# Optimization experiments

Hardware: AMD Instinct MI355X
Metric: run time of the kernel (lower is better)

Reference implementation:

```python
import jax, jax.numpy as jnp
import numpy as np

B, T, D, U = 32, 2048, 1024, 1024


def setup_inputs() -> dict:
    key = jax.random.key(0)
    ks = jax.random.split(key, 6)
    scale = 0.02
    return {
        "query": jax.random.normal(ks[0], (B, D), jnp.float32),
        "values": jax.random.normal(ks[1], (B, T, D), jnp.float32),
        "W1_k": jax.random.normal(ks[2], (D, U), jnp.float32) * scale,
        "W1_b": jnp.zeros((U,), jnp.float32),
        "W2_k": jax.random.normal(ks[3], (D, U), jnp.float32) * scale,
        "W2_b": jnp.zeros((U,), jnp.float32),
        "V_k": jax.random.normal(ks[4], (U, 1), jnp.float32) * scale,
        "V_b": jnp.zeros((1,), jnp.float32),
    }


def reference(query, values, W1_k, W1_b, W2_k, W2_b, V_k, V_b):
    # query: [B, D] -> [B, 1, U]; values: [B, T, D] -> [B, T, U]
    q_proj = (query @ W1_k + W1_b)[:, None, :]
    v_proj = jnp.einsum("btd,du->btu", values, W2_k) + W2_b
    # score: [B, T, 1]
    score = jnp.tanh(q_proj + v_proj) @ V_k + V_b
    attention_weights = jax.nn.softmax(score, axis=1)  # over time axis T
    context_vector = jnp.sum(attention_weights * values, axis=1)  # [B, D]
    return context_vector
```

## Files before the change

### kernel.cpp

```cpp
#include <hip/hip_runtime.h>

#define NB 32
#define NT 2048
#define ND 1024
#define NU 1024
#define NM (NB*NT)

using f32x4 = __attribute__((ext_vector_type(4))) float;
using s16x8 = __attribute__((ext_vector_type(8))) short;

#define BAR()   asm volatile("s_barrier" ::: "memory")
#define LGKM0() asm volatile("s_waitcnt lgkmcnt(0)" ::: "memory")
#define VMC(n)  asm volatile("s_waitcnt vmcnt(" #n ")" ::: "memory")
#define SB0()   __builtin_amdgcn_sched_barrier(0)

__device__ __forceinline__ unsigned short f2bf(float f) {
  unsigned u = __builtin_bit_cast(unsigned, f);
  u = u + 0x7fffu + ((u >> 16) & 1u);
  return (unsigned short)(u >> 16);
}

__device__ __forceinline__ unsigned cvtpk(float lo, float hi) {
  unsigned r;
  asm("v_cvt_pk_bf16_f32 %0, %1, %2" : "=v"(r) : "v"(lo), "v"(hi));
  return r;
}

__device__ __forceinline__ void gload_lds16(const void* g, void* l) {
  __builtin_amdgcn_global_load_lds(
      (const __attribute__((address_space(1))) unsigned int*)g,
      (__attribute__((address_space(3))) unsigned int*)l, 16, 0, 0);
}

__device__ __forceinline__ float tanh_fast(float x) {
  float e = __expf(2.0f * x);
  return 1.0f - 2.0f * __builtin_amdgcn_rcpf(e + 1.0f);
}

__device__ __forceinline__ void stage_half(const unsigned short* g, int gk,
                                           unsigned short* l, int w, int r3, int c8s) {
#pragma unroll
  for (int i = 0; i < 2; ++i) {
    int cb = i * 8 + w;
    gload_lds16(g + (((size_t)(cb * 8 + r3)) << 10) + gk + c8s * 8, l + cb * 512);
  }
}

__device__ __forceinline__ void load_halfA(const float* g, int kbase, int arow, int acol,
                                           float4 (&f)[4]) {
  const float* p = g + ((size_t)arow << 10) + kbase + acol * 16;
  f[0] = *(const float4*)(p);
  f[1] = *(const float4*)(p + 4);
  f[2] = *(const float4*)(p + 8);
  f[3] = *(const float4*)(p + 12);
}

__device__ __forceinline__ void cvt_half(const float4 (&f)[4], unsigned (&pk)[8]) {
  pk[0] = cvtpk(f[0].x, f[0].y); pk[1] = cvtpk(f[0].z, f[0].w);
  pk[2] = cvtpk(f[1].x, f[1].y); pk[3] = cvtpk(f[1].z, f[1].w);
  pk[4] = cvtpk(f[2].x, f[2].y); pk[5] = cvtpk(f[2].z, f[2].w);
  pk[6] = cvtpk(f[3].x, f[3].y); pk[7] = cvtpk(f[3].z, f[3].w);
}

__device__ __forceinline__ void write_half(const unsigned (&pk)[8], unsigned short* lds,
                                           int row, int acol) {
  int r7 = row & 7;
  int c0 = (acol * 2) ^ r7, c1 = (acol * 2 + 1) ^ r7;
  *(uint4*)(lds + (row << 6) + c0 * 8) = make_uint4(pk[0], pk[1], pk[2], pk[3]);
  *(uint4*)(lds + (row << 6) + c1 * 8) = make_uint4(pk[4], pk[5], pk[6], pk[7]);
}

#define MFMA_Q(MB, NB2) \
  _Pragma("unroll") \
  for (int m = 0; m < 4; ++m) { \
    _Pragma("unroll") \
    for (int n = 0; n < 2; ++n) { \
      _Pragma("unroll") \
      for (int ks = 0; ks < 2; ++ks) \
        acc[(MB) + m][(NB2) + n] = __builtin_amdgcn_mfma_f32_16x16x32_bf16( \
            fa[m][ks], fb[(NB2) + n][ks], acc[(MB) + m][(NB2) + n], 0, 0, 0); \
    } \
  }

template<bool ACVT, bool AISS, bool BST>
__device__ __forceinline__ void tile_body(
    int kt, int buf, const float* gA, const unsigned short* gB,
    unsigned short* sA, unsigned short* sB, f32x4 (&acc)[8][4], float4 (&ah)[2][4],
    int w, int wr, int wc, int l15, int lg, int r3, int c8s, int arow, int acol) {
  const unsigned short* pA = sA + buf * 16384;
  const unsigned short* pB = sB + buf * 16384;
  unsigned short* wA = sA + (buf ^ 1) * 16384;
  unsigned short* nB = sB + buf * 16384;
  const int l7 = l15 & 7;
  s16x8 fa[4][2], fb[4][2];
#pragma unroll
  for (int m = 0; m < 4; ++m)
#pragma unroll
    for (int ks = 0; ks < 2; ++ks)
      fa[m][ks] = *(const s16x8*)(pA + ((wr * 128 + m * 16 + l15) << 6) + (((ks * 4 + lg) ^ l7) << 3));
#pragma unroll
  for (int n = 0; n < 4; ++n)
#pragma unroll
    for (int ks = 0; ks < 2; ++ks)
      fb[n][ks] = *(const s16x8*)(pB + ((wc * 64 + n * 16 + l15) << 6) + (((ks * 4 + lg) ^ l7) << 3));
  BAR(); LGKM0(); SB0();
  __builtin_amdgcn_s_setprio(1); MFMA_Q(0, 0); __builtin_amdgcn_s_setprio(0);
  BAR();
  if (ACVT) {
    unsigned pk[8];
    cvt_half(ah[0], pk);
    write_half(pk, wA, arow, acol);
  }
  if (BST) stage_half(gB, (kt + 2) * 64, nB, w, r3, c8s);
  __builtin_amdgcn_s_setprio(1); MFMA_Q(0, 2); __builtin_amdgcn_s_setprio(0);
  LGKM0();
  BAR();
#pragma unroll
  for (int m = 0; m < 4; ++m)
#pragma unroll
    for (int ks = 0; ks < 2; ++ks)
      fa[m][ks] = *(const s16x8*)(pA + ((wr * 128 + (4 + m) * 16 + l15) << 6) + (((ks * 4 + lg) ^ l7) << 3));
  if (ACVT) {
    unsigned pk[8];
    cvt_half(ah[1], pk);
    write_half(pk, wA, 128 + arow, acol);
  }
  if (AISS) load_halfA(gA, (kt + 2) * 64, arow, acol, ah[0]);
  if (BST) stage_half(gB + (128 << 10), (kt + 2) * 64, nB + 8192, w, r3, c8s);
  LGKM0(); SB0();
  __builtin_amdgcn_s_setprio(1); MFMA_Q(4, 0); __builtin_amdgcn_s_setprio(0);
  BAR();
  if (AISS) load_halfA(gA + (128 << 10), (kt + 2) * 64, arow, acol, ah[1]);
  __builtin_amdgcn_s_setprio(1); MFMA_Q(4, 2); __builtin_amdgcn_s_setprio(0);
  BAR();
}

__global__ __launch_bounds__(512, 2) void k_score_gemm8(
    const float* __restrict__ values, const unsigned short* __restrict__ W2t,
    const float* __restrict__ add2, const float* __restrict__ Vk,
    float* __restrict__ score_part) {
  __shared__ unsigned short sA[32768];
  __shared__ unsigned short sB[32768];
  const int tid = threadIdx.x;
  const int w = tid >> 6, lane = tid & 63;
  const int wr = w >> 2, wc = w & 3;
  const int l15 = lane & 15, lg = lane >> 4;
  const int r3 = lane >> 3, c8s = (lane & 7) ^ r3;
  const int arow = tid >> 2, acol = tid & 3;

  const int L = blockIdx.x;
  const int g = (L & 7) * 128 + (L >> 3);
  const int mtile = g >> 2, ntile = g & 3;

  const float* gA = values + ((size_t)mtile << 18);
  const unsigned short* gB = W2t + ((size_t)ntile << 18);

  f32x4 acc[8][4] = {};
  float4 ah[2][4];

  {
    float4 f0[4], f1[4];
    unsigned p0[8], p1[8];
    load_halfA(gA, 0, arow, acol, f0);
    load_halfA(gA + (128 << 10), 0, arow, acol, f1);
    cvt_half(f0, p0); cvt_half(f1, p1);
    write_half(p0, sA, arow, acol);
    write_half(p1, sA, 128 + arow, acol);
    stage_half(gB, 0, sB, w, r3, c8s);
    stage_half(gB + (128 << 10), 0, sB + 8192, w, r3, c8s);
    stage_half(gB, 64, sB + 16384, w, r3, c8s);
    stage_half(gB + (128 << 10), 64, sB + 16384 + 8192, w, r3, c8s);
    load_halfA(gA, 64, arow, acol, ah[0]);
    load_halfA(gA + (128 << 10), 64, arow, acol, ah[1]);
    VMC(8);
    LGKM0();
    BAR();
  }

  int buf = 0;
  for (int kt = 0; kt < 14; ++kt) {
    tile_body<true, true, true>(kt, buf, gA, gB, sA, sB, acc, ah, w, wr, wc, l15, lg, r3, c8s, arow, acol);
    buf ^= 1;
  }
  tile_body<true, false, false>(14, buf, gA, gB, sA, sB, acc, ah, w, wr, wc, l15, lg, r3, c8s, arow, acol);
  buf ^= 1;
  tile_body<false, false, false>(15, buf, gA, gB, sA, sB, acc, ah, w, wr, wc, l15, lg, r3, c8s, arow, acol);

  const int b = (mtile * 256) >> 11;
  float vks[4], adds[4];
#pragma unroll
  for (int n = 0; n < 4; ++n) {
    int u = ntile * 256 + wc * 64 + n * 16 + l15;
    vks[n] = Vk[u];
    adds[n] = add2[(b << 10) + u];
  }
  __syncthreads();
  float* part = (float*)sA;
#pragma unroll
  for (int m = 0; m < 8; ++m) {
#pragma unroll
    for (int j = 0; j < 4; ++j) {
      float s = 0.f;
#pragma unroll
      for (int n = 0; n < 4; ++n) {
        float x = acc[m][n][j] + adds[n];
        s = fmaf(tanh_fast(x), vks[n], s);
      }
#pragma unroll
      for (int off = 1; off < 16; off <<= 1) s += __shfl_xor(s, off);
      if (l15 == 0) part[wc * 256 + wr * 128 + m * 16 + lg * 4 + j] = s;
    }
  }
  __syncthreads();
  if (tid < 256) {
    float v = part[tid] + part[256 + tid] + part[512 + tid] + part[768 + tid];
    score_part[((size_t)ntile << 16) + mtile * 256 + tid] = v;
  }
}

__global__ void k_qproj(const float* __restrict__ q, const float* __restrict__ W1,
                        const float* __restrict__ W1b, const float* __restrict__ W2b,
                        float* __restrict__ add2) {
  int u = blockIdx.x * 256 + threadIdx.x;
  int b = blockIdx.y;
  const float* qr = q + (b << 10);
  float s = 0.f;
#pragma unroll 8
  for (int d = 0; d < ND; ++d) s = fmaf(qr[d], W1[d * NU + u], s);
  add2[(b << 10) + u] = s + W1b[u] + W2b[u];
}

__global__ void k_w2t(const float* __restrict__ W2, unsigned short* __restrict__ W2t) {
  __shared__ unsigned short tile[64][65];
  int bu = blockIdx.x * 64, bd = blockIdx.y * 64;
  int x = threadIdx.x & 63, y4 = threadIdx.x >> 6;
#pragma unroll
  for (int r = 0; r < 16; ++r) {
    int dl = y4 * 16 + r;
    tile[x][dl] = f2bf(W2[(size_t)(bd + dl) * NU + bu + x]);
  }
  __syncthreads();
#pragma unroll
  for (int r = 0; r < 16; ++r) {
    int ul = y4 * 16 + r;
    W2t[(size_t)(bu + ul) * ND + bd + x] = tile[ul][x];
  }
}

__global__ void k_softmax(const float* __restrict__ sp, float* __restrict__ w) {
  __shared__ float redm[4], reds[4];
  int b = blockIdx.x, tid = threadIdx.x;
  float s[8];
  float mx = -1e30f;
#pragma unroll
  for (int i = 0; i < 8; ++i) {
    int t = i * 256 + tid;
    float v = 0.f;
#pragma unroll
    for (int p = 0; p < 4; ++p) v += sp[((size_t)p << 16) + (b << 11) + t];
    s[i] = v;
    mx = fmaxf(mx, v);
  }
#pragma unroll
  for (int o = 1; o < 64; o <<= 1) mx = fmaxf(mx, __shfl_xor(mx, o));
  if ((tid & 63) == 0) redm[tid >> 6] = mx;
  __syncthreads();
  mx = fmaxf(fmaxf(redm[0], redm[1]), fmaxf(redm[2], redm[3]));
  float sum = 0.f;
#pragma unroll
  for (int i = 0; i < 8; ++i) { s[i] = __expf(s[i] - mx); sum += s[i]; }
#pragma unroll
  for (int o = 1; o < 64; o <<= 1) sum += __shfl_xor(sum, o);
  if ((tid & 63) == 0) reds[tid >> 6] = sum;
  __syncthreads();
  float inv = 1.0f / (reds[0] + reds[1] + reds[2] + reds[3]);
#pragma unroll
  for (int i = 0; i < 8; ++i) w[(b << 11) + i * 256 + tid] = s[i] * inv;
}

__global__ void k_context(const float* __restrict__ values, const float* __restrict__ wv,
                          float* __restrict__ part) {
  int d4 = threadIdx.x;
  int b = blockIdx.y, tc = blockIdx.z;
  const float4* vb = (const float4*)(values + ((size_t)b << 21) + ((size_t)tc << 18)) + d4;
  const float* wb = wv + (b << 11) + (tc << 8);
  float ax = 0.f, ay = 0.f, az = 0.f, aw = 0.f;
#pragma unroll 4
  for (int t = 0; t < 256; ++t) {
    float4 v = vb[(size_t)t << 8];
    float wt = wb[t];
    ax = fmaf(wt, v.x, ax); ay = fmaf(wt, v.y, ay);
    az = fmaf(wt, v.z, az); aw = fmaf(wt, v.w, aw);
  }
  float4* po = (float4*)(part + (((size_t)tc * NB + b) << 10)) + d4;
  *po = make_float4(ax, ay, az, aw);
}

__global__ void k_ctx_reduce(const float* __restrict__ part, float* __restrict__ out) {
  int i = blockIdx.x * 256 + threadIdx.x;
  float s = 0.f;
#pragma unroll
  for (int p = 0; p < 8; ++p) s += part[(p << 15) + i];
  out[i] = s;
}

extern "C" void kernel_launch(void* const* d_in, const int* in_sizes, int n_in,
                              void* d_out, int out_size, void* d_ws, size_t ws_size,
                              hipStream_t stream) {
  const float* query  = (const float*)d_in[0];
  const float* values = (const float*)d_in[1];
  const float* W1k    = (const float*)d_in[2];
  const float* W1b    = (const float*)d_in[3];
  const float* W2k    = (const float*)d_in[4];
  const float* W2b    = (const float*)d_in[5];
  const float* Vk     = (const float*)d_in[6];
  float* out = (float*)d_out;
  char* ws = (char*)d_ws;

  size_t off = 0;
  float* add2 = (float*)(ws + off); off += (size_t)NB * NU * 4;
  float* sp   = (float*)(ws + off); off += (size_t)4 * NM * 4;
  float* wv   = (float*)(ws + off); off += (size_t)NM * 4;
  float* ctxp = (float*)(ws + off); off += (size_t)8 * NB * ND * 4;
  unsigned short* W2t = (unsigned short*)(ws + off); off += (size_t)NU * ND * 2;

  k_qproj<<<dim3(4, 32), 256, 0, stream>>>(query, W1k, W1b, W2b, add2);
  k_w2t<<<dim3(16, 16), 256, 0, stream>>>(W2k, W2t);
  k_score_gemm8<<<dim3(1024), 512, 0, stream>>>(values, W2t, add2, Vk, sp);
  k_softmax<<<dim3(32), 256, 0, stream>>>(sp, wv);
  k_context<<<dim3(1, 32, 8), 256, 0, stream>>>(values, wv, ctxp);
  k_ctx_reduce<<<dim3(128), 256, 0, stream>>>(ctxp, out);
}
```

Baseline: 298.2 us.

## Stage fp32 A tiles directly to LDS with 4-deep pipeline and smaller tiles

The score GEMM now streams fp32 values straight into LDS with global_load_lds and converts them to bf16 when reading MFMA fragments, instead of loading into registers, converting and writing bf16 into LDS. The tile shrinks from 256x256 to 128x256 with K-step 32 and a 4-stage ring buffer, and fragments for the next step are prefetched into double-buffered registers. The grid doubles to 2048 blocks. This aims to remove the register round-trip and VALU conversion stalls from the load path. In exchange it doubles the LDS bytes for A, repeats the bf16 conversion per wave that reads a fragment, and lowers per-block reuse of the B tile.

```diff
diff --git a/kernel.cpp b/kernel.cpp
--- a/kernel.cpp
+++ b/kernel.cpp
@@ -10,7 +10,6 @@
 using s16x8 = __attribute__((ext_vector_type(8))) short;
 
 #define BAR()   asm volatile("s_barrier" ::: "memory")
-#define LGKM0() asm volatile("s_waitcnt lgkmcnt(0)" ::: "memory")
 #define VMC(n)  asm volatile("s_waitcnt vmcnt(" #n ")" ::: "memory")
 #define SB0()   __builtin_amdgcn_sched_barrier(0)
 
@@ -37,156 +36,115 @@
   return 1.0f - 2.0f * __builtin_amdgcn_rcpf(e + 1.0f);
 }
 
-__device__ __forceinline__ void stage_half(const unsigned short* g, int gk,
-                                           unsigned short* l, int w, int r3, int c8s) {
+__device__ __forceinline__ void stageA(const float* g, float* l, int w, int lane) {
+  int rloc = lane >> 3;
+  int gc = (lane & 7) ^ rloc;
 #pragma unroll
   for (int i = 0; i < 2; ++i) {
-    int cb = i * 8 + w;
-    gload_lds16(g + (((size_t)(cb * 8 + r3)) << 10) + gk + c8s * 8, l + cb * 512);
-  }
-}
-
-__device__ __forceinline__ void load_halfA(const float* g, int kbase, int arow, int acol,
-                                           float4 (&f)[4]) {
-  const float* p = g + ((size_t)arow << 10) + kbase + acol * 16;
-  f[0] = *(const float4*)(p);
-  f[1] = *(const float4*)(p + 4);
-  f[2] = *(const float4*)(p + 8);
-  f[3] = *(const float4*)(p + 12);
-}
-
-__device__ __forceinline__ void cvt_half(const float4 (&f)[4], unsigned (&pk)[8]) {
-  pk[0] = cvtpk(f[0].x, f[0].y); pk[1] = cvtpk(f[0].z, f[0].w);
-  pk[2] = cvtpk(f[1].x, f[1].y); pk[3] = cvtpk(f[1].z, f[1].w);
-  pk[4] = cvtpk(f[2].x, f[2].y); pk[5] = cvtpk(f[2].z, f[2].w);
-  pk[6] = cvtpk(f[3].x, f[3].y); pk[7] = cvtpk(f[3].z, f[3].w);
-}
-
-__device__ __forceinline__ void write_half(const unsigned (&pk)[8], unsigned short* lds,
-                                           int row, int acol) {
+    int rb = (w * 2 + i) * 8;
+    gload_lds16(g + (size_t)(rb + rloc) * 1024 + gc * 4, l + rb * 32);
+  }
+}
+
+__device__ __forceinline__ void stageB(const unsigned short* g, unsigned short* l,
+                                       int w, int lane) {
+  int l2 = lane >> 2;
+  int gc = (lane & 3) ^ ((lane >> 3) & 3);
+#pragma unroll
+  for (int i = 0; i < 2; ++i) {
+    int rblk = w * 2 + i;
+    gload_lds16(g + (size_t)(rblk * 16 + l2) * 1024 + gc * 8, l + rblk * 512);
+  }
+}
+
+__device__ __forceinline__ s16x8 frag_read(const unsigned short* buf, int row, int lg) {
+  int cr = lg ^ ((row >> 1) & 3);
+  return *(const s16x8*)(buf + row * 32 + cr * 8);
+}
+
+__device__ __forceinline__ s16x8 fragA_f32(const float* buf, int row, int lg) {
   int r7 = row & 7;
-  int c0 = (acol * 2) ^ r7, c1 = (acol * 2 + 1) ^ r7;
-  *(uint4*)(lds + (row << 6) + c0 * 8) = make_uint4(pk[0], pk[1], pk[2], pk[3]);
-  *(uint4*)(lds + (row << 6) + c1 * 8) = make_uint4(pk[4], pk[5], pk[6], pk[7]);
-}
-
-#define MFMA_Q(MB, NB2) \
-  _Pragma("unroll") \
-  for (int m = 0; m < 4; ++m) { \
-    _Pragma("unroll") \
-    for (int n = 0; n < 2; ++n) { \
-      _Pragma("unroll") \
-      for (int ks = 0; ks < 2; ++ks) \
-        acc[(MB) + m][(NB2) + n] = __builtin_amdgcn_mfma_f32_16x16x32_bf16( \
-            fa[m][ks], fb[(NB2) + n][ks], acc[(MB) + m][(NB2) + n], 0, 0, 0); \
-    } \
-  }
-
-template<bool ACVT, bool AISS, bool BST>
-__device__ __forceinline__ void tile_body(
-    int kt, int buf, const float* gA, const unsigned short* gB,
-    unsigned short* sA, unsigned short* sB, f32x4 (&acc)[8][4], float4 (&ah)[2][4],
-    int w, int wr, int wc, int l15, int lg, int r3, int c8s, int arow, int acol) {
-  const unsigned short* pA = sA + buf * 16384;
-  const unsigned short* pB = sB + buf * 16384;
-  unsigned short* wA = sA + (buf ^ 1) * 16384;
-  unsigned short* nB = sB + buf * 16384;
-  const int l7 = l15 & 7;
-  s16x8 fa[4][2], fb[4][2];
+  int c0 = (lg * 2) ^ r7, c1 = (lg * 2 + 1) ^ r7;
+  f32x4 x = *(const f32x4*)(buf + row * 32 + c0 * 4);
+  f32x4 y = *(const f32x4*)(buf + row * 32 + c1 * 4);
+  uint4 u = make_uint4(cvtpk(x[0], x[1]), cvtpk(x[2], x[3]),
+                       cvtpk(y[0], y[1]), cvtpk(y[2], y[3]));
+  return __builtin_bit_cast(s16x8, u);
+}
+
+template<bool PRE, bool ST, int VM>
+__device__ __forceinline__ void tile_one(
+    int kt, const float* gA, const unsigned short* gB,
+    float* sAf, unsigned short* sB, f32x4 (&acc)[4][4],
+    s16x8 (&fa)[4], s16x8 (&fb)[4], s16x8 (&nfa)[4], s16x8 (&nfb)[4],
+    int w, int lane, int wr, int wc, int l15, int lg) {
+  if constexpr (VM == 4) { VMC(4); }
+  else if constexpr (VM == 0) { VMC(0); }
+  BAR();
+  if (ST) {
+    stageA(gA + (size_t)(kt + 3) * 32, sAf + ((kt + 3) & 3) * 4096, w, lane);
+    stageB(gB + (size_t)(kt + 3) * 32, sB + ((kt + 3) & 3) * 8192, w, lane);
+  }
+  if (PRE) {
+    const float* qA = sAf + ((kt + 1) & 3) * 4096;
+    const unsigned short* qB = sB + ((kt + 1) & 3) * 8192;
+#pragma unroll
+    for (int i = 0; i < 4; ++i) nfa[i] = fragA_f32(qA, wr * 64 + i * 16 + l15, lg);
+#pragma unroll
+    for (int n = 0; n < 4; ++n) nfb[n] = frag_read(qB, wc * 64 + n * 16 + l15, lg);
+  }
+  SB0();
+  __builtin_amdgcn_s_setprio(1);
 #pragma unroll
   for (int m = 0; m < 4; ++m)
 #pragma unroll
-    for (int ks = 0; ks < 2; ++ks)
-      fa[m][ks] = *(const s16x8*)(pA + ((wr * 128 + m * 16 + l15) << 6) + (((ks * 4 + lg) ^ l7) << 3));
-#pragma unroll
-  for (int n = 0; n < 4; ++n)
-#pragma unroll
-    for (int ks = 0; ks < 2; ++ks)
-      fb[n][ks] = *(const s16x8*)(pB + ((wc * 64 + n * 16 + l15) << 6) + (((ks * 4 + lg) ^ l7) << 3));
-  BAR(); LGKM0(); SB0();
-  __builtin_amdgcn_s_setprio(1); MFMA_Q(0, 0); __builtin_amdgcn_s_setprio(0);
-  BAR();
-  if (ACVT) {
-    unsigned pk[8];
-    cvt_half(ah[0], pk);
-    write_half(pk, wA, arow, acol);
-  }
-  if (BST) stage_half(gB, (kt + 2) * 64, nB, w, r3, c8s);
-  __builtin_amdgcn_s_setprio(1); MFMA_Q(0, 2); __builtin_amdgcn_s_setprio(0);
-  LGKM0();
-  BAR();
-#pragma unroll
-  for (int m = 0; m < 4; ++m)
-#pragma unroll
-    for (int ks = 0; ks < 2; ++ks)
-      fa[m][ks] = *(const s16x8*)(pA + ((wr * 128 + (4 + m) * 16 + l15) << 6) + (((ks * 4 + lg) ^ l7) << 3));
-  if (ACVT) {
-    unsigned pk[8];
-    cvt_half(ah[1], pk);
-    write_half(pk, wA, 128 + arow, acol);
-  }
-  if (AISS) load_halfA(gA, (kt + 2) * 64, arow, acol, ah[0]);
-  if (BST) stage_half(gB + (128 << 10), (kt + 2) * 64, nB + 8192, w, r3, c8s);
-  LGKM0(); SB0();
-  __builtin_amdgcn_s_setprio(1); MFMA_Q(4, 0); __builtin_amdgcn_s_setprio(0);
-  BAR();
-  if (AISS) load_halfA(gA + (128 << 10), (kt + 2) * 64, arow, acol, ah[1]);
-  __builtin_amdgcn_s_setprio(1); MFMA_Q(4, 2); __builtin_amdgcn_s_setprio(0);
-  BAR();
-}
-
-__global__ __launch_bounds__(512, 2) void k_score_gemm8(
+    for (int n = 0; n < 4; ++n)
+      acc[m][n] = __builtin_amdgcn_mfma_f32_16x16x32_bf16(fa[m], fb[n], acc[m][n], 0, 0, 0);
+  __builtin_amdgcn_s_setprio(0);
+}
+
+__global__ __launch_bounds__(512, 2) void k_score_gemmf(
     const float* __restrict__ values, const unsigned short* __restrict__ W2t,
     const float* __restrict__ add2, const float* __restrict__ Vk,
     float* __restrict__ score_part) {
-  __shared__ unsigned short sA[32768];
+  __shared__ float sAf[16384];
   __shared__ unsigned short sB[32768];
   const int tid = threadIdx.x;
   const int w = tid >> 6, lane = tid & 63;
   const int wr = w >> 2, wc = w & 3;
   const int l15 = lane & 15, lg = lane >> 4;
-  const int r3 = lane >> 3, c8s = (lane & 7) ^ r3;
-  const int arow = tid >> 2, acol = tid & 3;
 
   const int L = blockIdx.x;
-  const int g = (L & 7) * 128 + (L >> 3);
+  const int g = (L & 7) * 256 + (L >> 3);
   const int mtile = g >> 2, ntile = g & 3;
 
-  const float* gA = values + ((size_t)mtile << 18);
+  const float* gA = values + ((size_t)mtile << 17);
   const unsigned short* gB = W2t + ((size_t)ntile << 18);
 
-  f32x4 acc[8][4] = {};
-  float4 ah[2][4];
-
-  {
-    float4 f0[4], f1[4];
-    unsigned p0[8], p1[8];
-    load_halfA(gA, 0, arow, acol, f0);
-    load_halfA(gA + (128 << 10), 0, arow, acol, f1);
-    cvt_half(f0, p0); cvt_half(f1, p1);
-    write_half(p0, sA, arow, acol);
-    write_half(p1, sA, 128 + arow, acol);
-    stage_half(gB, 0, sB, w, r3, c8s);
-    stage_half(gB + (128 << 10), 0, sB + 8192, w, r3, c8s);
-    stage_half(gB, 64, sB + 16384, w, r3, c8s);
-    stage_half(gB + (128 << 10), 64, sB + 16384 + 8192, w, r3, c8s);
-    load_halfA(gA, 64, arow, acol, ah[0]);
-    load_halfA(gA + (128 << 10), 64, arow, acol, ah[1]);
-    VMC(8);
-    LGKM0();
-    BAR();
-  }
-
-  int buf = 0;
-  for (int kt = 0; kt < 14; ++kt) {
-    tile_body<true, true, true>(kt, buf, gA, gB, sA, sB, acc, ah, w, wr, wc, l15, lg, r3, c8s, arow, acol);
-    buf ^= 1;
-  }
-  tile_body<true, false, false>(14, buf, gA, gB, sA, sB, acc, ah, w, wr, wc, l15, lg, r3, c8s, arow, acol);
-  buf ^= 1;
-  tile_body<false, false, false>(15, buf, gA, gB, sA, sB, acc, ah, w, wr, wc, l15, lg, r3, c8s, arow, acol);
-
-  const int b = (mtile * 256) >> 11;
+  f32x4 acc[4][4] = {};
+  s16x8 fa0[4], fb0[4], fa1[4], fb1[4];
+
+  stageA(gA, sAf, w, lane);                   stageB(gB, sB, w, lane);
+  stageA(gA + 32, sAf + 4096, w, lane);       stageB(gB + 32, sB + 8192, w, lane);
+  stageA(gA + 64, sAf + 8192, w, lane);       stageB(gB + 64, sB + 16384, w, lane);
+  VMC(8);
+  BAR();
+#pragma unroll
+  for (int i = 0; i < 4; ++i) fa0[i] = fragA_f32(sAf, wr * 64 + i * 16 + l15, lg);
+#pragma unroll
+  for (int n = 0; n < 4; ++n) fb0[n] = frag_read(sB, wc * 64 + n * 16 + l15, lg);
+
+#pragma unroll 1
+  for (int kt = 0; kt < 28; kt += 2) {
+    tile_one<true, true, 4>(kt,     gA, gB, sAf, sB, acc, fa0, fb0, fa1, fb1, w, lane, wr, wc, l15, lg);
+    tile_one<true, true, 4>(kt + 1, gA, gB, sAf, sB, acc, fa1, fb1, fa0, fb0, w, lane, wr, wc, l15, lg);
+  }
+  tile_one<true,  true,  4>(28, gA, gB, sAf, sB, acc, fa0, fb0, fa1, fb1, w, lane, wr, wc, l15, lg);
+  tile_one<true,  false, 4>(29, gA, gB, sAf, sB, acc, fa1, fb1, fa0, fb0, w, lane, wr, wc, l15, lg);
+  tile_one<true,  false, 0>(30, gA, gB, sAf, sB, acc, fa0, fb0, fa1, fb1, w, lane, wr, wc, l15, lg);
+  tile_one<false, false,-1>(31, gA, gB, sAf, sB, acc, fa1, fb1, fa0, fb0, w, lane, wr, wc, l15, lg);
+
+  const int b = mtile >> 4;
   float vks[4], adds[4];
 #pragma unroll
   for (int n = 0; n < 4; ++n) {
@@ -195,9 +153,9 @@
     adds[n] = add2[(b << 10) + u];
   }
   __syncthreads();
-  float* part = (float*)sA;
-#pragma unroll
-  for (int m = 0; m < 8; ++m) {
+  float* part = (float*)sAf;
+#pragma unroll
+  for (int m = 0; m < 4; ++m) {
 #pragma unroll
     for (int j = 0; j < 4; ++j) {
       float s = 0.f;
@@ -208,13 +166,13 @@
       }
 #pragma unroll
       for (int off = 1; off < 16; off <<= 1) s += __shfl_xor(s, off);
-      if (l15 == 0) part[wc * 256 + wr * 128 + m * 16 + lg * 4 + j] = s;
+      if (l15 == 0) part[wc * 128 + wr * 64 + m * 16 + lg * 4 + j] = s;
     }
   }
   __syncthreads();
-  if (tid < 256) {
-    float v = part[tid] + part[256 + tid] + part[512 + tid] + part[768 + tid];
-    score_part[((size_t)ntile << 16) + mtile * 256 + tid] = v;
+  if (tid < 128) {
+    float v = part[tid] + part[128 + tid] + part[256 + tid] + part[384 + tid];
+    score_part[((size_t)ntile << 16) + mtile * 128 + tid] = v;
   }
 }
 
@@ -326,7 +284,7 @@
 
   k_qproj<<<dim3(4, 32), 256, 0, stream>>>(query, W1k, W1b, W2b, add2);
   k_w2t<<<dim3(16, 16), 256, 0, stream>>>(W2k, W2t);
-  k_score_gemm8<<<dim3(1024), 512, 0, stream>>>(values, W2t, add2, Vk, sp);
+  k_score_gemmf<<<dim3(2048), 512, 0, stream>>>(values, W2t, add2, Vk, sp);
   k_softmax<<<dim3(32), 256, 0, stream>>>(sp, wv);
   k_context<<<dim3(1, 32, 8), 256, 0, stream>>>(values, wv, ctxp);
   k_ctx_reduce<<<dim3(128), 256, 0, stream>>>(ctxp, out);
```

Result: slower. 405.3 us (+35.9%).
